# Performance work log

Hardware: AMD Instinct MI355X
Metric: run time of the kernel (lower is better)

## Reference

```python
import jax, jax.numpy as jnp
import numpy as np

EPS = 0.1

def setup_inputs() -> dict:
    key = jax.random.key(0)
    k1, k2, k3, k4, k5, k6 = jax.random.split(key, 6)
    B, N, Cin, Cout = 8, 2048, 128, 128
    x = jax.random.normal(k1, (B, N, Cin), dtype=jnp.float32)
    x_0 = jax.random.normal(k2, (B, N, Cout), dtype=jnp.float32)
    adj = jax.random.randint(k3, (B, N, N), 0, 2, dtype=jnp.int32)
    # learned parameters (Linear without bias stores weight [out,in]; we keep [in,out])
    W_lin = jax.random.normal(k4, (Cin, Cout), dtype=jnp.float32) / np.sqrt(Cin)
    w_att_l = jax.random.normal(k5, (Cout,), dtype=jnp.float32) / np.sqrt(Cout)
    w_att_r = jax.random.normal(k6, (Cout,), dtype=jnp.float32) / np.sqrt(Cout)
    return {"x": x, "x_0": x_0, "adj": adj, "W_lin": W_lin, "w_att_l": w_att_l, "w_att_r": w_att_r}

def reference(x, x_0, adj, W_lin, w_att_l, w_att_r):
    # x: [B,N,Cin] -> h: [B,N,Cout]
    h = jnp.einsum('bni,io->bno', x, W_lin)
    alpha_l = jnp.einsum('bno,o->bn', h, w_att_l)  # [B,N]
    alpha_r = jnp.einsum('bno,o->bn', h, w_att_r)  # [B,N]
    # alpha[b,i,j] = tanh(alpha_r[b,i] * alpha_l[b,j])
    alpha = jnp.tanh(alpha_r[:, :, None] * alpha_l[:, None, :])  # [B,N,N]
    alpha = jnp.where(adj == 0, jnp.float32(0.0), alpha)
    # dropout p=0.0 -> identity
    out = jnp.einsum('bij,bjo->bio', alpha, h)  # [B,N,Cout]
    return out + EPS * x_0
```

## Files before the change

### kernel.cpp

```cpp
#include <hip/hip_runtime.h>
#include <stdint.h>

#define B_   8
#define N_   2048
#define C_   128
#define EPS_ 0.1f

typedef __attribute__((ext_vector_type(8))) short short8;
typedef __attribute__((ext_vector_type(4))) float f32x4;

__device__ __forceinline__ unsigned short f2bf(float f) {
    union { float f; uint32_t u; } v; v.f = f;
    uint32_t u = v.u + 0x7FFF + ((v.u >> 16) & 1);
    return (unsigned short)(u >> 16);
}

__global__ __launch_bounds__(128) void k_wt(const float* __restrict__ W,
                                            unsigned short* __restrict__ Wt) {
    const int o = blockIdx.x, k = threadIdx.x;
    Wt[o * C_ + k] = f2bf(W[k * C_ + o]);
}

__global__ __launch_bounds__(256) void k_h(
    const float* __restrict__ x, const unsigned short* __restrict__ Wt,
    const float* __restrict__ wl, const float* __restrict__ wr,
    unsigned short* __restrict__ ht, float* __restrict__ al, float* __restrict__ ar)
{
    const int b    = blockIdx.x >> 5;
    const int i0   = (blockIdx.x & 31) * 64;
    const int t    = threadIdx.x;
    const int lane = t & 63;
    const int wid  = t >> 6;

    __shared__ __align__(16) unsigned short xs[64 * 128];
    __shared__ __align__(16) unsigned short ws[128 * 128];

    #pragma unroll
    for (int p = 0; p < 4; ++p) {
        const int s = p * 256 + t, row = s >> 4, u = s & 15;
        const float* gp = x + ((size_t)(b * N_ + i0 + row) * C_ + u * 8);
        float4 f0 = *(const float4*)gp;
        float4 f1 = *(const float4*)(gp + 4);
        short8 tv;
        tv[0] = (short)f2bf(f0.x); tv[1] = (short)f2bf(f0.y);
        tv[2] = (short)f2bf(f0.z); tv[3] = (short)f2bf(f0.w);
        tv[4] = (short)f2bf(f1.x); tv[5] = (short)f2bf(f1.y);
        tv[6] = (short)f2bf(f1.z); tv[7] = (short)f2bf(f1.w);
        *(short8*)&xs[row * 128 + (u ^ (row & 15)) * 8] = tv;
    }
    #pragma unroll
    for (int p = 0; p < 8; ++p) {
        const int s = p * 256 + t, o = s >> 4, u = s & 15;
        int4 v = *(const int4*)(Wt + o * C_ + u * 8);
        *(int4*)&ws[o * 128 + (u ^ (o & 15)) * 8] = v;
    }
    __syncthreads();

    const int m0 = wid * 16, lr = lane & 15, q = lane >> 4;
    f32x4 acc[8];
    #pragma unroll
    for (int i = 0; i < 8; ++i) acc[i] = (f32x4){0.f, 0.f, 0.f, 0.f};

    #pragma unroll
    for (int s = 0; s < 4; ++s) {
        const int m = m0 + lr;
        short8 af = *(const short8*)&xs[m * 128 + ((s * 4 + q) ^ (m & 15)) * 8];
        #pragma unroll
        for (int tt = 0; tt < 8; ++tt) {
            const int o = tt * 16 + lr;
            short8 bf = *(const short8*)&ws[o * 128 + ((s * 4 + q) ^ (o & 15)) * 8];
            acc[tt] = __builtin_amdgcn_mfma_f32_16x16x32_bf16(af, bf, acc[tt], 0, 0, 0);
        }
    }

    float pl[4] = {0.f, 0.f, 0.f, 0.f}, pr[4] = {0.f, 0.f, 0.f, 0.f};
    const int j0 = i0 + m0 + q * 4;
    #pragma unroll
    for (int tt = 0; tt < 8; ++tt) {
        const int o = tt * 16 + lr;
        const float wlv = wl[o], wrv = wr[o];
        unsigned int lo = (unsigned int)f2bf(acc[tt][0]) | ((unsigned int)f2bf(acc[tt][1]) << 16);
        unsigned int hi = (unsigned int)f2bf(acc[tt][2]) | ((unsigned int)f2bf(acc[tt][3]) << 16);
        uint2 u2; u2.x = lo; u2.y = hi;
        *(uint2*)&ht[((size_t)(b * C_ + o)) * N_ + j0] = u2;
        #pragma unroll
        for (int r = 0; r < 4; ++r) {
            pl[r] = fmaf(acc[tt][r], wlv, pl[r]);
            pr[r] = fmaf(acc[tt][r], wrv, pr[r]);
        }
    }
    #pragma unroll
    for (int msk = 1; msk < 16; msk <<= 1) {
        #pragma unroll
        for (int r = 0; r < 4; ++r) {
            pl[r] += __shfl_xor(pl[r], msk, 64);
            pr[r] += __shfl_xor(pr[r], msk, 64);
        }
    }
    if (lr == 0) {
        #pragma unroll
        for (int r = 0; r < 4; ++r) {
            al[b * N_ + j0 + r] = pl[r];
            ar[b * N_ + j0 + r] = pr[r];
        }
    }
}

struct Pref {
    int4   a[4];
    float4 l[4];
    int4   hb[8];
};

__global__ __launch_bounds__(256) void k_out(
    const int* __restrict__ adj, const unsigned short* __restrict__ ht,
    const float* __restrict__ al, const float* __restrict__ ar,
    const float* __restrict__ x0, float* __restrict__ out)
{
    const int b    = blockIdx.x >> 6;
    const int i0   = (blockIdx.x & 63) * 32;
    const int t    = threadIdx.x;
    const int lane = t & 63;
    const int wid  = t >> 6;

    const int m0 = (wid & 1) * 16, n0 = (wid >> 1) * 64;
    const int lr = lane & 15, q = lane >> 4;
    const int q8 = q * 8;

    const int irow = i0 + m0 + lr;
    const float arv = ar[b * N_ + irow];
    const float tl  = 2.f * arv;
    const int*            adjp = adj + ((size_t)(b * N_) + irow) * N_;
    const float*          alp  = al + b * N_;
    const unsigned short* hbp  = ht + ((size_t)(b * C_) + n0 + lr) * N_;

    auto ldc = [&](int c) -> Pref {
        Pref P;
        const int j0 = c * 64 + q8;
        #pragma unroll
        for (int s2 = 0; s2 < 2; ++s2) {
            P.a[s2 * 2]     = *(const int4*)(adjp + j0 + s2 * 32);
            P.a[s2 * 2 + 1] = *(const int4*)(adjp + j0 + s2 * 32 + 4);
            P.l[s2 * 2]     = *(const float4*)(alp + j0 + s2 * 32);
            P.l[s2 * 2 + 1] = *(const float4*)(alp + j0 + s2 * 32 + 4);
            #pragma unroll
            for (int tt = 0; tt < 4; ++tt)
                P.hb[s2 * 4 + tt] =
                    *(const int4*)(hbp + (size_t)(tt * 16) * N_ + j0 + s2 * 32);
        }
        return P;
    };

    f32x4 acc[4];
    #pragma unroll
    for (int i = 0; i < 4; ++i) acc[i] = (f32x4){0.f, 0.f, 0.f, 0.f};

    auto cmp = [&](const Pref& P) {
        #pragma unroll
        for (int s2 = 0; s2 < 2; ++s2) {
            const int*   av = (const int*)&P.a[s2 * 2];
            const float* lv = (const float*)&P.l[s2 * 2];
            short8 af;
            #pragma unroll
            for (int e = 0; e < 8; ++e) {
                float ex = __expf(tl * lv[e]);
                float th = 1.f - 2.f / (ex + 1.f);
                af[e] = av[e] ? (short)f2bf(th) : (short)0;
            }
            #pragma unroll
            for (int tt = 0; tt < 4; ++tt) {
                short8 bf = *(const short8*)&P.hb[s2 * 4 + tt];
                acc[tt] = __builtin_amdgcn_mfma_f32_16x16x32_bf16(af, bf, acc[tt], 0, 0, 0);
            }
        }
    };

    Pref PA = ldc(0);
    #pragma unroll 1
    for (int c = 0; c < 32; c += 2) {
        Pref PB = ldc(c + 1);
        cmp(PA);
        if (c + 2 < 32) PA = ldc(c + 2);
        cmp(PB);
    }

    #pragma unroll
    for (int tt = 0; tt < 4; ++tt) {
        const int o = n0 + tt * 16 + lr;
        #pragma unroll
        for (int r = 0; r < 4; ++r) {
            const int row = i0 + m0 + q * 4 + r;
            const size_t idx = ((size_t)(b * N_) + row) * C_ + o;
            out[idx] = acc[tt][r] + EPS_ * x0[idx];
        }
    }
}

extern "C" void kernel_launch(void* const* d_in, const int* in_sizes, int n_in,
                              void* d_out, int out_size, void* d_ws, size_t ws_size,
                              hipStream_t stream) {
    const float* x   = (const float*)d_in[0];
    const float* x0  = (const float*)d_in[1];
    const int*   adj = (const int*)d_in[2];
    const float* W   = (const float*)d_in[3];
    const float* wl  = (const float*)d_in[4];
    const float* wr  = (const float*)d_in[5];
    float* out = (float*)d_out;

    unsigned short* ht = (unsigned short*)d_ws;
    float* al = (float*)((char*)d_ws + (size_t)B_ * C_ * N_ * 2);
    float* ar = al + B_ * N_;
    unsigned short* Wt = (unsigned short*)(ar + B_ * N_);

    k_wt <<<C_,             C_,  0, stream>>>(W, Wt);
    k_h  <<<B_ * (N_ / 64), 256, 0, stream>>>(x, Wt, wl, wr, ht, al, ar);
    k_out<<<B_ * (N_ / 32), 256, 0, stream>>>(adj, ht, al, ar, x0, out);
}
```

Baseline: 270.3 us.

## Compute masked tanh attention tile once per block via shared memory

In the earlier kernel, each wave recomputed the tanh/mask A-fragment for its 16 rows, so the two waves sharing the same rows but different output columns duplicated the exp, divide and adjacency loads. Now all 256 threads cooperatively compute the 32x64 bf16 alpha tile once per chunk and store it in a double-buffered, swizzled LDS buffer that the MFMA waves read. The change also uses a hardware reciprocal instead of a divide, sets launch bounds to two blocks per CU, and deepens the prefetch of adj/alpha_l and h. In exchange it adds two block barriers per chunk pair and LDS traffic.

```diff
diff --git a/kernel.cpp b/kernel.cpp
--- a/kernel.cpp
+++ b/kernel.cpp
@@ -106,13 +106,15 @@
     }
 }
 
-struct Pref {
-    int4   a[4];
-    float4 l[4];
-    int4   hb[8];
+struct SD {
+    int4   a0, a1;
+    float4 l0, l1;
 };
-
-__global__ __launch_bounds__(256) void k_out(
+struct HB {
+    int4 h[8];
+};
+
+__global__ __launch_bounds__(256, 2) void k_out(
     const int* __restrict__ adj, const unsigned short* __restrict__ ht,
     const float* __restrict__ al, const float* __restrict__ ar,
     const float* __restrict__ x0, float* __restrict__ out)
@@ -123,65 +125,94 @@
     const int lane = t & 63;
     const int wid  = t >> 6;
 
+    __shared__ __align__(16) unsigned short a_s[2][32 * 64];
+
+    const int arow = t >> 3;
+    const int jq   = t & 7;
+    const float arv = ar[b * N_ + i0 + arow];
+    const float tl  = 2.f * arv;
+    const int*   adjp = adj + ((size_t)(b * N_) + i0 + arow) * N_ + jq * 8;
+    const float* alp  = al + b * N_ + jq * 8;
+
+    auto ld_sd = [&](int c) -> SD {
+        SD P;
+        const int j0 = c * 64;
+        P.a0 = *(const int4*)(adjp + j0);
+        P.a1 = *(const int4*)(adjp + j0 + 4);
+        P.l0 = *(const float4*)(alp + j0);
+        P.l1 = *(const float4*)(alp + j0 + 4);
+        return P;
+    };
+
+    auto stage = [&](int buf, const SD& P) {
+        short8 pk;
+        const int*   av = (const int*)&P.a0;
+        const float* lv = (const float*)&P.l0;
+        #pragma unroll
+        for (int e = 0; e < 8; ++e) {
+            float ex = __expf(tl * lv[e]);
+            float th = 1.f - 2.f * __builtin_amdgcn_rcpf(ex + 1.f);
+            pk[e] = av[e] ? (short)f2bf(th) : (short)0;
+        }
+        const int su = (jq ^ (arow & 7)) * 8;
+        *(short8*)&a_s[buf][arow * 64 + su] = pk;
+    };
+
     const int m0 = (wid & 1) * 16, n0 = (wid >> 1) * 64;
     const int lr = lane & 15, q = lane >> 4;
-    const int q8 = q * 8;
-
-    const int irow = i0 + m0 + lr;
-    const float arv = ar[b * N_ + irow];
-    const float tl  = 2.f * arv;
-    const int*            adjp = adj + ((size_t)(b * N_) + irow) * N_;
-    const float*          alp  = al + b * N_;
-    const unsigned short* hbp  = ht + ((size_t)(b * C_) + n0 + lr) * N_;
-
-    auto ldc = [&](int c) -> Pref {
-        Pref P;
-        const int j0 = c * 64 + q8;
-        #pragma unroll
-        for (int s2 = 0; s2 < 2; ++s2) {
-            P.a[s2 * 2]     = *(const int4*)(adjp + j0 + s2 * 32);
-            P.a[s2 * 2 + 1] = *(const int4*)(adjp + j0 + s2 * 32 + 4);
-            P.l[s2 * 2]     = *(const float4*)(alp + j0 + s2 * 32);
-            P.l[s2 * 2 + 1] = *(const float4*)(alp + j0 + s2 * 32 + 4);
+    const unsigned short* hbp = ht + ((size_t)(b * C_) + n0 + lr) * N_ + q * 8;
+
+    auto ld_hb = [&](int c) -> HB {
+        HB H;
+        const int j0 = c * 64;
+        #pragma unroll
+        for (int s2 = 0; s2 < 2; ++s2)
             #pragma unroll
             for (int tt = 0; tt < 4; ++tt)
-                P.hb[s2 * 4 + tt] =
+                H.h[s2 * 4 + tt] =
                     *(const int4*)(hbp + (size_t)(tt * 16) * N_ + j0 + s2 * 32);
-        }
-        return P;
+        return H;
     };
 
     f32x4 acc[4];
     #pragma unroll
     for (int i = 0; i < 4; ++i) acc[i] = (f32x4){0.f, 0.f, 0.f, 0.f};
 
-    auto cmp = [&](const Pref& P) {
+    auto mma = [&](int buf, const HB& H) {
         #pragma unroll
         for (int s2 = 0; s2 < 2; ++s2) {
-            const int*   av = (const int*)&P.a[s2 * 2];
-            const float* lv = (const float*)&P.l[s2 * 2];
-            short8 af;
-            #pragma unroll
-            for (int e = 0; e < 8; ++e) {
-                float ex = __expf(tl * lv[e]);
-                float th = 1.f - 2.f / (ex + 1.f);
-                af[e] = av[e] ? (short)f2bf(th) : (short)0;
-            }
+            const int m = m0 + lr;
+            short8 afr = *(const short8*)&a_s[buf][m * 64 + ((s2 * 4 + q) ^ (m & 7)) * 8];
             #pragma unroll
             for (int tt = 0; tt < 4; ++tt) {
-                short8 bf = *(const short8*)&P.hb[s2 * 4 + tt];
-                acc[tt] = __builtin_amdgcn_mfma_f32_16x16x32_bf16(af, bf, acc[tt], 0, 0, 0);
+                short8 bfr = *(const short8*)&H.h[s2 * 4 + tt];
+                acc[tt] = __builtin_amdgcn_mfma_f32_16x16x32_bf16(afr, bfr, acc[tt], 0, 0, 0);
             }
         }
     };
 
-    Pref PA = ldc(0);
-    #pragma unroll 1
-    for (int c = 0; c < 32; c += 2) {
-        Pref PB = ldc(c + 1);
-        cmp(PA);
-        if (c + 2 < 32) PA = ldc(c + 2);
-        cmp(PB);
+    SD sd0 = ld_sd(0);
+    SD sdA = ld_sd(1);
+    SD sdB = ld_sd(2);
+    HB hb0 = ld_hb(0);
+    HB hb1 = ld_hb(1);
+    stage(0, sd0);
+    __syncthreads();
+
+    for (int cc = 0; cc < 16; ++cc) {
+        stage(1, sdA);
+        if (cc < 15) sdA = ld_sd(2 * cc + 3);
+        mma(0, hb0);
+        if (cc < 15) hb0 = ld_hb(2 * cc + 2);
+        __syncthreads();
+
+        if (cc < 15) {
+            stage(0, sdB);
+            if (cc < 14) sdB = ld_sd(2 * cc + 4);
+        }
+        mma(1, hb1);
+        if (cc < 15) hb1 = ld_hb(2 * cc + 3);
+        __syncthreads();
     }
 
     #pragma unroll
```

New measurement: 240.6 us. 11.0% less time.

## Stage masked tanh tile through per-wave LDS with deeper adj prefetch pipeline

Applied to the files above, without the earlier changes.

Each lane now computes a contiguous 16-element chunk of the masked tanh row, using a fast reciprocal instead of division. It writes the chunk into a double-buffered, swizzled per-wave LDS tile, and the MFMA A-fragments are read back from there. The adjacency loads are prefetched up to four chunks ahead, separately from the al and h loads, and launch bounds request two blocks per CU. The goal is better coalesced adj reads and longer memory-latency hiding, at the cost of LDS traffic, extra registers for the deeper prefetch, and the lack of explicit barriers within the wave between buffer reuse.

```diff
diff --git a/kernel.cpp b/kernel.cpp
--- a/kernel.cpp
+++ b/kernel.cpp
@@ -106,13 +106,11 @@
     }
 }
 
-struct Pref {
-    int4   a[4];
-    float4 l[4];
-    int4   hb[8];
-};
-
-__global__ __launch_bounds__(256) void k_out(
+struct AdjC { int4   a[4]; };
+struct AlC  { float4 f[4]; };
+struct HbC  { int4   h[8]; };
+
+__global__ __launch_bounds__(256, 2) void k_out(
     const int* __restrict__ adj, const unsigned short* __restrict__ ht,
     const float* __restrict__ al, const float* __restrict__ ar,
     const float* __restrict__ x0, float* __restrict__ out)
@@ -124,74 +122,125 @@
     const int wid  = t >> 6;
 
     const int m0 = (wid & 1) * 16, n0 = (wid >> 1) * 64;
+
+    __shared__ __align__(16) unsigned short a_s[4][2][16 * 64];
+    unsigned short* wls = &a_s[wid][0][0];
+
+    const int r = lane >> 2, g = lane & 3;
+    const float arv = ar[b * N_ + i0 + m0 + r];
+    const float tl  = 2.f * arv;
+    const int*   adjp = adj + ((size_t)(b * N_) + i0 + m0 + r) * N_ + g * 16;
+    const float* alp  = al + b * N_ + g * 16;
+
+    auto ld_adj = [&](int c) -> AdjC {
+        AdjC A; const int j0 = (c & 31) * 64;
+        #pragma unroll
+        for (int k = 0; k < 4; ++k) A.a[k] = *(const int4*)(adjp + j0 + k * 4);
+        return A;
+    };
+    auto ld_al = [&](int c) -> AlC {
+        AlC L; const int j0 = (c & 31) * 64;
+        #pragma unroll
+        for (int k = 0; k < 4; ++k) L.f[k] = *(const float4*)(alp + j0 + k * 4);
+        return L;
+    };
+
+    auto stage = [&](int buf, const AdjC& A, const AlC& L) {
+        const int*   av = (const int*)&A.a[0];
+        const float* lv = (const float*)&L.f[0];
+        short8 p0, p1;
+        #pragma unroll
+        for (int e = 0; e < 8; ++e) {
+            float ex = __expf(tl * lv[e]);
+            float th = 1.f - 2.f * __builtin_amdgcn_rcpf(ex + 1.f);
+            p0[e] = av[e] ? (short)f2bf(th) : (short)0;
+        }
+        #pragma unroll
+        for (int e = 0; e < 8; ++e) {
+            float ex = __expf(tl * lv[8 + e]);
+            float th = 1.f - 2.f * __builtin_amdgcn_rcpf(ex + 1.f);
+            p1[e] = av[8 + e] ? (short)f2bf(th) : (short)0;
+        }
+        unsigned short* wp = wls + buf * 1024 + r * 64;
+        *(short8*)&wp[((g * 2    ) ^ (r & 7)) * 8] = p0;
+        *(short8*)&wp[((g * 2 + 1) ^ (r & 7)) * 8] = p1;
+    };
+
     const int lr = lane & 15, q = lane >> 4;
-    const int q8 = q * 8;
-
-    const int irow = i0 + m0 + lr;
-    const float arv = ar[b * N_ + irow];
-    const float tl  = 2.f * arv;
-    const int*            adjp = adj + ((size_t)(b * N_) + irow) * N_;
-    const float*          alp  = al + b * N_;
-    const unsigned short* hbp  = ht + ((size_t)(b * C_) + n0 + lr) * N_;
-
-    auto ldc = [&](int c) -> Pref {
-        Pref P;
-        const int j0 = c * 64 + q8;
-        #pragma unroll
-        for (int s2 = 0; s2 < 2; ++s2) {
-            P.a[s2 * 2]     = *(const int4*)(adjp + j0 + s2 * 32);
-            P.a[s2 * 2 + 1] = *(const int4*)(adjp + j0 + s2 * 32 + 4);
-            P.l[s2 * 2]     = *(const float4*)(alp + j0 + s2 * 32);
-            P.l[s2 * 2 + 1] = *(const float4*)(alp + j0 + s2 * 32 + 4);
+    const unsigned short* hbp = ht + ((size_t)(b * C_) + n0 + lr) * N_ + q * 8;
+
+    auto ld_hb = [&](int c) -> HbC {
+        HbC H; const int j0 = (c & 31) * 64;
+        #pragma unroll
+        for (int s2 = 0; s2 < 2; ++s2)
             #pragma unroll
             for (int tt = 0; tt < 4; ++tt)
-                P.hb[s2 * 4 + tt] =
+                H.h[s2 * 4 + tt] =
                     *(const int4*)(hbp + (size_t)(tt * 16) * N_ + j0 + s2 * 32);
-        }
-        return P;
+        return H;
     };
 
     f32x4 acc[4];
     #pragma unroll
     for (int i = 0; i < 4; ++i) acc[i] = (f32x4){0.f, 0.f, 0.f, 0.f};
 
-    auto cmp = [&](const Pref& P) {
+    auto mma = [&](int buf, const HbC& H) {
+        const unsigned short* rp = wls + buf * 1024 + lr * 64;
         #pragma unroll
         for (int s2 = 0; s2 < 2; ++s2) {
-            const int*   av = (const int*)&P.a[s2 * 2];
-            const float* lv = (const float*)&P.l[s2 * 2];
-            short8 af;
-            #pragma unroll
-            for (int e = 0; e < 8; ++e) {
-                float ex = __expf(tl * lv[e]);
-                float th = 1.f - 2.f / (ex + 1.f);
-                af[e] = av[e] ? (short)f2bf(th) : (short)0;
-            }
+            short8 afr = *(const short8*)&rp[((s2 * 4 + q) ^ (lr & 7)) * 8];
             #pragma unroll
             for (int tt = 0; tt < 4; ++tt) {
-                short8 bf = *(const short8*)&P.hb[s2 * 4 + tt];
-                acc[tt] = __builtin_amdgcn_mfma_f32_16x16x32_bf16(af, bf, acc[tt], 0, 0, 0);
+                short8 bfr = *(const short8*)&H.h[s2 * 4 + tt];
+                acc[tt] = __builtin_amdgcn_mfma_f32_16x16x32_bf16(afr, bfr, acc[tt], 0, 0, 0);
             }
         }
     };
 
-    Pref PA = ldc(0);
+    AdjC adjA, adjB, adjC_, adjD;
+    AlC  alA, alB;
+    HbC  hbA, hbB;
+    {
+        AdjC a0 = ld_adj(0); AlC l0 = ld_al(0);
+        adjA = ld_adj(1); adjB = ld_adj(2); adjC_ = ld_adj(3); adjD = ld_adj(4);
+        alA  = ld_al(1);  alB  = ld_al(2);
+        hbA  = ld_hb(0);  hbB  = ld_hb(1);
+        stage(0, a0, l0);
+    }
+
     #pragma unroll 1
-    for (int c = 0; c < 32; c += 2) {
-        Pref PB = ldc(c + 1);
-        cmp(PA);
-        if (c + 2 < 32) PA = ldc(c + 2);
-        cmp(PB);
+    for (int k = 0; k < 8; ++k) {
+        const int c0 = k * 4;
+
+        stage(1, adjA, alA);
+        adjA = ld_adj(c0 + 5); alA = ld_al(c0 + 3);
+        mma(0, hbA);
+        hbA = ld_hb(c0 + 2);
+
+        stage(0, adjB, alB);
+        adjB = ld_adj(c0 + 6); alB = ld_al(c0 + 4);
+        mma(1, hbB);
+        hbB = ld_hb(c0 + 3);
+
+        stage(1, adjC_, alA);
+        adjC_ = ld_adj(c0 + 7); alA = ld_al(c0 + 5);
+        mma(0, hbA);
+        hbA = ld_hb(c0 + 4);
+
+        if (k < 7) stage(0, adjD, alB);
+        adjD = ld_adj(c0 + 8); alB = ld_al(c0 + 6);
+        mma(1, hbB);
+        hbB = ld_hb(c0 + 5);
     }
 
     #pragma unroll
     for (int tt = 0; tt < 4; ++tt) {
         const int o = n0 + tt * 16 + lr;
         #pragma unroll
-        for (int r = 0; r < 4; ++r) {
-            const int row = i0 + m0 + q * 4 + r;
+        for (int rr = 0; rr < 4; ++rr) {
+            const int row = i0 + m0 + q * 4 + rr;
             const size_t idx = ((size_t)(b * N_) + row) * C_ + o;
-            out[idx] = acc[tt][r] + EPS_ * x0[idx];
+            out[idx] = acc[tt][rr] + EPS_ * x0[idx];
         }
     }
 }
```

Measured after the change: 273.7 us. No clear change (+1.3%).

## Restructure k_out to single-wave 16-row blocks covering all 128 output columns

Applied to the files above, without the earlier changes.

Each block of k_out is now one wavefront that computes 16 rows across all 128 output channels, instead of four waves splitting 32 rows by two column halves. Each alpha tile (the tanh of the outer product with the adjacency mask) is now computed once per row and used for all columns, so the recomputation across column-split waves goes away. The adjacency and al values are prefetched two chunks ahead, and the division is replaced with a hardware reciprocal. In exchange, each wave holds more registers (8 accumulators and 16 h vectors), and since h is now loaded directly per chunk rather than prefetched, its memory latency may be exposed.

```diff
diff --git a/kernel.cpp b/kernel.cpp
--- a/kernel.cpp
+++ b/kernel.cpp
@@ -106,90 +106,108 @@
     }
 }
 
-struct Pref {
-    int4   a[4];
-    float4 l[4];
-    int4   hb[8];
-};
-
-__global__ __launch_bounds__(256) void k_out(
+struct AdjC { int4   a[4]; };
+struct AlC  { float4 f[4]; };
+struct HbC  { int4   h[16]; };
+
+__global__ __launch_bounds__(64, 2) void k_out(
     const int* __restrict__ adj, const unsigned short* __restrict__ ht,
     const float* __restrict__ al, const float* __restrict__ ar,
     const float* __restrict__ x0, float* __restrict__ out)
 {
-    const int b    = blockIdx.x >> 6;
-    const int i0   = (blockIdx.x & 63) * 32;
-    const int t    = threadIdx.x;
-    const int lane = t & 63;
-    const int wid  = t >> 6;
-
-    const int m0 = (wid & 1) * 16, n0 = (wid >> 1) * 64;
-    const int lr = lane & 15, q = lane >> 4;
-    const int q8 = q * 8;
-
-    const int irow = i0 + m0 + lr;
-    const float arv = ar[b * N_ + irow];
+    const int b    = blockIdx.x & 7;
+    const int i0   = (blockIdx.x >> 3) * 16;
+    const int lane = threadIdx.x;
+    const int lr   = lane & 15, q = lane >> 4;
+
+    const float arv = ar[b * N_ + i0 + lr];
     const float tl  = 2.f * arv;
-    const int*            adjp = adj + ((size_t)(b * N_) + irow) * N_;
-    const float*          alp  = al + b * N_;
-    const unsigned short* hbp  = ht + ((size_t)(b * C_) + n0 + lr) * N_;
-
-    auto ldc = [&](int c) -> Pref {
-        Pref P;
-        const int j0 = c * 64 + q8;
+
+    const int*            adjp = adj + ((size_t)(b * N_) + i0 + lr) * N_ + q * 8;
+    const float*          alp  = al + b * N_ + q * 8;
+    const unsigned short* htp  = ht + ((size_t)(b * C_) + lr) * N_ + q * 8;
+
+    auto ld_adj = [&](int c) -> AdjC {
+        AdjC A; const int j0 = c * 64;
         #pragma unroll
         for (int s2 = 0; s2 < 2; ++s2) {
-            P.a[s2 * 2]     = *(const int4*)(adjp + j0 + s2 * 32);
-            P.a[s2 * 2 + 1] = *(const int4*)(adjp + j0 + s2 * 32 + 4);
-            P.l[s2 * 2]     = *(const float4*)(alp + j0 + s2 * 32);
-            P.l[s2 * 2 + 1] = *(const float4*)(alp + j0 + s2 * 32 + 4);
+            A.a[s2 * 2]     = *(const int4*)(adjp + j0 + s2 * 32);
+            A.a[s2 * 2 + 1] = *(const int4*)(adjp + j0 + s2 * 32 + 4);
+        }
+        return A;
+    };
+    auto ld_al = [&](int c) -> AlC {
+        AlC L; const int j0 = c * 64;
+        #pragma unroll
+        for (int s2 = 0; s2 < 2; ++s2) {
+            L.f[s2 * 2]     = *(const float4*)(alp + j0 + s2 * 32);
+            L.f[s2 * 2 + 1] = *(const float4*)(alp + j0 + s2 * 32 + 4);
+        }
+        return L;
+    };
+    auto ld_hb = [&](int c) -> HbC {
+        HbC H; const int j0 = c * 64;
+        #pragma unroll
+        for (int s2 = 0; s2 < 2; ++s2)
             #pragma unroll
-            for (int tt = 0; tt < 4; ++tt)
-                P.hb[s2 * 4 + tt] =
-                    *(const int4*)(hbp + (size_t)(tt * 16) * N_ + j0 + s2 * 32);
-        }
-        return P;
-    };
-
-    f32x4 acc[4];
-    #pragma unroll
-    for (int i = 0; i < 4; ++i) acc[i] = (f32x4){0.f, 0.f, 0.f, 0.f};
-
-    auto cmp = [&](const Pref& P) {
-        #pragma unroll
-        for (int s2 = 0; s2 < 2; ++s2) {
-            const int*   av = (const int*)&P.a[s2 * 2];
-            const float* lv = (const float*)&P.l[s2 * 2];
-            short8 af;
-            #pragma unroll
-            for (int e = 0; e < 8; ++e) {
-                float ex = __expf(tl * lv[e]);
-                float th = 1.f - 2.f / (ex + 1.f);
-                af[e] = av[e] ? (short)f2bf(th) : (short)0;
-            }
-            #pragma unroll
-            for (int tt = 0; tt < 4; ++tt) {
-                short8 bf = *(const short8*)&P.hb[s2 * 4 + tt];
-                acc[tt] = __builtin_amdgcn_mfma_f32_16x16x32_bf16(af, bf, acc[tt], 0, 0, 0);
-            }
-        }
-    };
-
-    Pref PA = ldc(0);
+            for (int tt = 0; tt < 8; ++tt)
+                H.h[s2 * 8 + tt] =
+                    *(const int4*)(htp + (size_t)(tt * 16) * N_ + j0 + s2 * 32);
+        return H;
+    };
+
+    auto alpha2 = [&](const AdjC& A, const AlC& L, int s2) -> short8 {
+        const int*   av = (const int*)&A.a[s2 * 2];
+        const float* lv = (const float*)&L.f[s2 * 2];
+        short8 pk;
+        #pragma unroll
+        for (int e = 0; e < 8; ++e) {
+            float ex = __expf(tl * lv[e]);
+            float th = 1.f - 2.f * __builtin_amdgcn_rcpf(ex + 1.f);
+            pk[e] = av[e] ? (short)f2bf(th) : (short)0;
+        }
+        return pk;
+    };
+
+    f32x4 acc[8];
+    #pragma unroll
+    for (int i = 0; i < 8; ++i) acc[i] = (f32x4){0.f, 0.f, 0.f, 0.f};
+
+    auto mma8 = [&](short8 f0, short8 f1, const HbC& H) {
+        #pragma unroll
+        for (int tt = 0; tt < 8; ++tt)
+            acc[tt] = __builtin_amdgcn_mfma_f32_16x16x32_bf16(
+                f0, *(const short8*)&H.h[tt], acc[tt], 0, 0, 0);
+        #pragma unroll
+        for (int tt = 0; tt < 8; ++tt)
+            acc[tt] = __builtin_amdgcn_mfma_f32_16x16x32_bf16(
+                f1, *(const short8*)&H.h[8 + tt], acc[tt], 0, 0, 0);
+    };
+
+    AdjC aA = ld_adj(0), aB = ld_adj(1);
+    AlC  lA = ld_al(0),  lB = ld_al(1);
+
     #pragma unroll 1
     for (int c = 0; c < 32; c += 2) {
-        Pref PB = ldc(c + 1);
-        cmp(PA);
-        if (c + 2 < 32) PA = ldc(c + 2);
-        cmp(PB);
-    }
-
-    #pragma unroll
-    for (int tt = 0; tt < 4; ++tt) {
-        const int o = n0 + tt * 16 + lr;
-        #pragma unroll
-        for (int r = 0; r < 4; ++r) {
-            const int row = i0 + m0 + q * 4 + r;
+        HbC hA = ld_hb(c);
+        short8 f0 = alpha2(aA, lA, 0);
+        short8 f1 = alpha2(aA, lA, 1);
+        if (c + 2 < 32) { aA = ld_adj(c + 2); lA = ld_al(c + 2); }
+        mma8(f0, f1, hA);
+
+        HbC hB = ld_hb(c + 1);
+        short8 g0 = alpha2(aB, lB, 0);
+        short8 g1 = alpha2(aB, lB, 1);
+        if (c + 3 < 32) { aB = ld_adj(c + 3); lB = ld_al(c + 3); }
+        mma8(g0, g1, hB);
+    }
+
+    #pragma unroll
+    for (int tt = 0; tt < 8; ++tt) {
+        const int o = tt * 16 + lr;
+        #pragma unroll
+        for (int r = 0; r < 4; ++r) {
+            const int row = i0 + q * 4 + r;
             const size_t idx = ((size_t)(b * N_) + row) * C_ + o;
             out[idx] = acc[tt][r] + EPS_ * x0[idx];
         }
@@ -214,5 +232,5 @@
 
     k_wt <<<C_,             C_,  0, stream>>>(W, Wt);
     k_h  <<<B_ * (N_ / 64), 256, 0, stream>>>(x, Wt, wl, wr, ht, al, ar);
-    k_out<<<B_ * (N_ / 32), 256, 0, stream>>>(adj, ht, al, ar, x0, out);
-}
+    k_out<<<B_ * (N_ / 16), 64,  0, stream>>>(adj, ht, al, ar, x0, out);
+}
```

Result: faster. 255.1 us (-5.6%).
